# Performance work log

Measured on AMD Instinct MI355X. Metric: run time of the kernel, lower is better.

The kernel has to match this reference:

```python
import jax, jax.numpy as jnp
import numpy as np

B, S, D = 2, 2048, 4096
NQ, NKV, DK = 32, 4, 128
GROUPS = NQ // NKV  # 8
NEG = -1e9  # finite stand-in for -inf so fully-masked rows stay NaN-free


def setup_inputs() -> dict:
    key = jax.random.key(0)
    ks = jax.random.split(key, 5)
    return {
        "x": jax.random.normal(ks[0], (B, S, D), jnp.float32),
        "Wq": jax.random.normal(ks[1], (D, NQ * DK), jnp.float32) * 0.02,
        "Wk": jax.random.normal(ks[2], (D, NKV * DK), jnp.float32) * 0.02,
        "Wv": jax.random.normal(ks[3], (D, NKV * DK), jnp.float32) * 0.02,
        "Wo": jax.random.normal(ks[4], (NQ * DK, D), jnp.float32) * 0.02,
    }


def reference(x, Wq, Wk, Wv, Wo):
    b, s, _ = x.shape
    # projections -> [b, heads, s, dk]
    Q = (x @ Wq).reshape(b, s, NQ, DK).transpose(0, 2, 1, 3)
    K = (x @ Wk).reshape(b, s, NKV, DK).transpose(0, 2, 1, 3)
    V = (x @ Wv).reshape(b, s, NKV, DK).transpose(0, 2, 1, 3)
    # GQA: repeat_interleave KV heads to match Q heads
    K = jnp.repeat(K, GROUPS, axis=1)  # [b, NQ, s, dk]
    V = jnp.repeat(V, GROUPS, axis=1)
    scores = jnp.einsum("bhqd,bhkd->bhqk", Q, K) / np.sqrt(DK).astype(np.float32)
    # faithful to source: mask = triu(ones(s, kv_len), diag=kv_len-s+1); fill where mask==0
    mask = jnp.triu(jnp.ones((s, s), jnp.float32), k=1)
    scores = jnp.where(mask == 0, NEG, scores)
    attn = jax.nn.softmax(scores, axis=-1)  # dropout = identity (eval)
    out = jnp.einsum("bhqk,bhkd->bhqd", attn, V)
    out = out.transpose(0, 2, 1, 3).reshape(b, s, NQ * DK)
    return out @ Wo
```

## Files before the change

kernel.cpp:

```cpp
#include <hip/hip_runtime.h>
#include <hip/hip_bf16.h>

#define S_LEN 2048
#define DMODEL 4096
#define NQH 32
#define NKVH 4
#define DKH 128

typedef __attribute__((ext_vector_type(8))) short bf16x8;
typedef __attribute__((ext_vector_type(4))) float f32x4;
typedef __attribute__((ext_vector_type(16))) float f32x16;
typedef __attribute__((ext_vector_type(2))) unsigned u32x2;

union PU { unsigned u[4]; bf16x8 v; };

__device__ __forceinline__ float b2f(short u) {
  union { float f; unsigned int i; } cv;
  cv.i = ((unsigned int)(unsigned short)u) << 16;
  return cv.f;
}

__device__ __forceinline__ unsigned cvt_pk(float lo, float hi) {
  unsigned r;
  asm("v_cvt_pk_bf16_f32 %0, %1, %2" : "=v"(r) : "v"(lo), "v"(hi));
  return r;
}

__device__ __forceinline__ void gload16(const void* g, void* l) {
  __builtin_amdgcn_global_load_lds(
      (const __attribute__((address_space(1))) void*)g,
      (__attribute__((address_space(3))) void*)l, 16, 0, 0);
}

#define BAR()                         \
  {                                   \
    asm volatile("" ::: "memory");    \
    __builtin_amdgcn_s_barrier();     \
    asm volatile("" ::: "memory");    \
  }

__global__ __launch_bounds__(256) void cast_kernel(
    const float* __restrict__ in, __hip_bfloat16* __restrict__ out, int n4) {
  for (int i = blockIdx.x * 256 + threadIdx.x; i < n4; i += gridDim.x * 256) {
    const float4 v = reinterpret_cast<const float4*>(in)[i];
    __hip_bfloat16 t[4] = {__float2bfloat16(v.x), __float2bfloat16(v.y),
                           __float2bfloat16(v.z), __float2bfloat16(v.w)};
    reinterpret_cast<uint2*>(out)[i] = *reinterpret_cast<const uint2*>(t);
  }
}

__device__ __forceinline__ void transpose_tile(const float* __restrict__ W,
                                               __hip_bfloat16* __restrict__ WT,
                                               int K, int N, int n0, int k0,
                                               int tid,
                                               __hip_bfloat16 (*tile)[64]) {
#pragma unroll
  for (int i = 0; i < 2; ++i) {
    const int fid = i * 256 + tid;
    const int r = fid >> 3, cc = fid & 7;
    const float4 v0 = *reinterpret_cast<const float4*>(
        &W[(size_t)(k0 + r) * N + n0 + cc * 8]);
    const float4 v1 = *reinterpret_cast<const float4*>(
        &W[(size_t)(k0 + r) * N + n0 + cc * 8 + 4]);
    __hip_bfloat16 t[8] = {__float2bfloat16(v0.x), __float2bfloat16(v0.y),
                           __float2bfloat16(v0.z), __float2bfloat16(v0.w),
                           __float2bfloat16(v1.x), __float2bfloat16(v1.y),
                           __float2bfloat16(v1.z), __float2bfloat16(v1.w)};
    *reinterpret_cast<bf16x8*>(&tile[r][(cc ^ (r & 7)) << 3]) =
        *reinterpret_cast<const bf16x8*>(t);
  }
  __syncthreads();
  const int n = tid >> 2, kw = tid & 3;
#pragma unroll
  for (int i = 0; i < 2; ++i) {
    const int kc = kw + i * 4;
    __hip_bfloat16 t[8];
#pragma unroll
    for (int j = 0; j < 8; ++j) {
      const int r = kc * 8 + j;
      t[j] = tile[r][((((n >> 3) ^ (r & 7)) << 3)) + (n & 7)];
    }
    *reinterpret_cast<bf16x8*>(&WT[(size_t)(n0 + n) * K + k0 + kc * 8]) =
        *reinterpret_cast<const bf16x8*>(t);
  }
}

__global__ __launch_bounds__(256) void transpose_cast_kernel(
    const float* __restrict__ W, __hip_bfloat16* __restrict__ WT, int K, int N) {
  __shared__ __align__(16) __hip_bfloat16 tile[64][64];
  transpose_tile(W, WT, K, N, blockIdx.x * 64, blockIdx.y * 64, threadIdx.x,
                 tile);
}

__global__ __launch_bounds__(256) void transpose_kv_kernel(
    const float* __restrict__ Wk, const float* __restrict__ Wv,
    __hip_bfloat16* __restrict__ KVT) {
  __shared__ __align__(16) __hip_bfloat16 tile[64][64];
  const int half = blockIdx.x >> 3;
  const float* W = half ? Wv : Wk;
  __hip_bfloat16* WT = KVT + (size_t)half * 512 * 4096;
  transpose_tile(W, WT, 4096, 512, (blockIdx.x & 7) * 64, blockIdx.y * 64,
                 threadIdx.x, tile);
}

template <int WMODE>
__global__ __launch_bounds__(512, 2) void gemm256(
    const __hip_bfloat16* __restrict__ A, const __hip_bfloat16* __restrict__ BT,
    void* __restrict__ C) {
  __shared__ __align__(16) char ldsA[131072];
  const char* lds = &ldsA[0];
  const int tid = threadIdx.x, lane = tid & 63, w = tid >> 6;
  const int l15 = lane & 15, g = lane >> 4;
  const int wr = w >> 2, wcn = w & 3;
  const int id = blockIdx.x;
  const int swz = (id & 7) * 32 + (id >> 3);
  const int bm = (swz >> 4) * 256, bn = (swz & 15) * 256;
  const int row0 = tid >> 3;
  const int kbg = ((tid & 7) * 16) ^ ((row0 & 7) << 4);
  const char* Ab = (const char*)A;
  const char* Bb = (const char*)BT;
  const size_t aR = (size_t)(bm + row0) * 8192 + kbg;
  const size_t bR = (size_t)(bn + row0) * 8192 + kbg;
  char* ldsw = const_cast<char*>(lds) + w * 1024;
  const int sw = (l15 & 7) << 4;
  const int okk = (g * 16) ^ sw;
  const int rA = (wr * 64 + l15) * 128;
  const int rB = (wcn * 32 + l15) * 128;

  f32x4 acc[8][4] = {};

#define STG2(XR, XB, DST)            \
  gload16(XB + (XR), ldsw + (DST));  \
  gload16(XB + (XR) + 524288, ldsw + (DST) + 8192)

  STG2(aR, Ab, 0);
  STG2(bR, Bb, 65536);
  STG2(aR + 1048576, Ab, 16384);
  STG2(bR + 1048576, Bb, 65536 + 16384);
  STG2(aR + 128, Ab, 32768);
  STG2(bR + 128, Bb, 65536 + 32768);

  for (int t = 0; t < 64; ++t) {
    const int pc = t & 1, pn = pc ^ 1;
    const int pA = pc * 32768, pB = 65536 + pc * 32768;
    const size_t s01 = (size_t)((t + 1 < 64) ? t + 1 : t - 1) * 128;
    const size_t s23 = (size_t)((t + 2 < 64) ? t + 2 : t) * 128;
    asm volatile("s_waitcnt vmcnt(4)" ::: "memory");
    BAR();
    bf16x8 a0[4][2], b0[2][2];
#pragma unroll
    for (int m = 0; m < 4; ++m)
#pragma unroll
      for (int kk = 0; kk < 2; ++kk)
        a0[m][kk] = *reinterpret_cast<const bf16x8*>(
            lds + pA + rA + m * 2048 + (okk ^ (kk << 6)));
#pragma unroll
    for (int n = 0; n < 2; ++n)
#pragma unroll
      for (int kk = 0; kk < 2; ++kk)
        b0[n][kk] = *reinterpret_cast<const bf16x8*>(
            lds + pB + rB + n * 2048 + (okk ^ (kk << 6)));
    STG2(aR + 1048576 + s01, Ab, pn * 32768 + 16384);
    __builtin_amdgcn_s_setprio(1);
#pragma unroll
    for (int kk = 0; kk < 2; ++kk)
#pragma unroll
      for (int m = 0; m < 4; ++m)
#pragma unroll
        for (int n = 0; n < 2; ++n)
          acc[m][n] = __builtin_amdgcn_mfma_f32_16x16x32_bf16(
              a0[m][kk], b0[n][kk], acc[m][n], 0, 0, 0);
    __builtin_amdgcn_s_setprio(0);
    bf16x8 b1[2][2];
#pragma unroll
    for (int n = 0; n < 2; ++n)
#pragma unroll
      for (int kk = 0; kk < 2; ++kk)
        b1[n][kk] = *reinterpret_cast<const bf16x8*>(
            lds + pB + 16384 + rB + n * 2048 + (okk ^ (kk << 6)));
    STG2(bR + 1048576 + s01, Bb, 65536 + pn * 32768 + 16384);
    BAR();
    __builtin_amdgcn_s_setprio(1);
#pragma unroll
    for (int kk = 0; kk < 2; ++kk)
#pragma unroll
      for (int m = 0; m < 4; ++m)
#pragma unroll
        for (int n = 0; n < 2; ++n)
          acc[m][2 + n] = __builtin_amdgcn_mfma_f32_16x16x32_bf16(
              a0[m][kk], b1[n][kk], acc[m][2 + n], 0, 0, 0);
    __builtin_amdgcn_s_setprio(0);
    bf16x8 a1[4][2];
#pragma unroll
    for (int m = 0; m < 4; ++m)
#pragma unroll
      for (int kk = 0; kk < 2; ++kk)
        a1[m][kk] = *reinterpret_cast<const bf16x8*>(
            lds + pA + 16384 + rA + m * 2048 + (okk ^ (kk << 6)));
    STG2(aR + s23, Ab, pc * 32768);
    __builtin_amdgcn_s_setprio(1);
#pragma unroll
    for (int kk = 0; kk < 2; ++kk)
#pragma unroll
      for (int m = 0; m < 4; ++m)
#pragma unroll
        for (int n = 0; n < 2; ++n)
          acc[4 + m][n] = __builtin_amdgcn_mfma_f32_16x16x32_bf16(
              a1[m][kk], b0[n][kk], acc[4 + m][n], 0, 0, 0);
    __builtin_amdgcn_s_setprio(0);
    STG2(bR + s23, Bb, 65536 + pc * 32768);
    __builtin_amdgcn_s_setprio(1);
#pragma unroll
    for (int kk = 0; kk < 2; ++kk)
#pragma unroll
      for (int m = 0; m < 4; ++m)
#pragma unroll
        for (int n = 0; n < 2; ++n)
          acc[4 + m][2 + n] = __builtin_amdgcn_mfma_f32_16x16x32_bf16(
              a1[m][kk], b1[n][kk], acc[4 + m][2 + n], 0, 0, 0);
    __builtin_amdgcn_s_setprio(0);
  }
  asm volatile("s_waitcnt vmcnt(0)" ::: "memory");

  const int crow0 = bm + wr * 64 + g * 4;
  const int ccol0 = bn + wcn * 32 + l15;
#pragma unroll
  for (int M = 0; M < 8; ++M)
#pragma unroll
    for (int N = 0; N < 4; ++N) {
      const int row = crow0 + (M >> 2) * 128 + (M & 3) * 16;
      const int col = ccol0 + (N >> 1) * 128 + (N & 1) * 16;
#pragma unroll
      for (int r = 0; r < 4; ++r) {
        if constexpr (WMODE == 0)
          ((float*)C)[(size_t)(row + r) * 4096 + col] = acc[M][N][r];
        else
          ((__hip_bfloat16*)C)[(size_t)(row + r) * 4096 + col] =
              __float2bfloat16(acc[M][N][r]);
      }
    }
}

__global__ __launch_bounds__(256) void gemm_kv(
    const __hip_bfloat16* __restrict__ A, const __hip_bfloat16* __restrict__ BT,
    __hip_bfloat16* __restrict__ Kb, __hip_bfloat16* __restrict__ VT) {
  __shared__ __align__(16) __hip_bfloat16 As[64 * 32];
  __shared__ __align__(16) __hip_bfloat16 Bs[128 * 32];
  const int tid = threadIdx.x, lane = tid & 63, w = tid >> 6;
  const int l15 = lane & 15, l4 = lane >> 4;
  const int bm = blockIdx.y * 64, bn = blockIdx.x * 128;
  const int wr = (w >> 1) * 32, wc = (w & 1) * 64;
  const int srow = lane >> 2, scol = (lane & 3) * 8;
  const __hip_bfloat16* ga = &A[(size_t)(bm + (tid >> 2)) * 4096 + scol];
  const __hip_bfloat16* gb = &BT[(size_t)(bn + w * 16 + srow) * 4096 + scol];
  char* laA = (char*)&As[0] + w * 1024;
  char* lb0 = (char*)&Bs[0] + w * 1024;
  char* lb1 = (char*)&Bs[0] + 4096 + w * 1024;
  f32x4 acc[2][4] = {};

  for (int k0 = 0; k0 < 4096; k0 += 32) {
    gload16(ga, laA);
    gload16(gb, lb0);
    gload16(gb + (size_t)64 * 4096, lb1);
    ga += 32;
    gb += 32;
    __syncthreads();
    bf16x8 af[2], bfr[4];
#pragma unroll
    for (int m = 0; m < 2; ++m)
      af[m] = *reinterpret_cast<const bf16x8*>(
          &As[(wr + m * 16 + l15) * 32 + l4 * 8]);
#pragma unroll
    for (int n = 0; n < 4; ++n)
      bfr[n] = *reinterpret_cast<const bf16x8*>(
          &Bs[(wc + n * 16 + l15) * 32 + l4 * 8]);
#pragma unroll
    for (int m = 0; m < 2; ++m)
#pragma unroll
      for (int n = 0; n < 4; ++n)
        acc[m][n] = __builtin_amdgcn_mfma_f32_16x16x32_bf16(af[m], bfr[n],
                                                            acc[m][n], 0, 0, 0);
    __syncthreads();
  }

#pragma unroll
  for (int m = 0; m < 2; ++m)
#pragma unroll
    for (int n = 0; n < 4; ++n) {
      const int row = bm + wr + m * 16 + l4 * 4;
      const int col = bn + wc + n * 16 + l15;
      if (col < 512) {
#pragma unroll
        for (int r = 0; r < 4; ++r)
          Kb[(size_t)(row + r) * 512 + col] = __float2bfloat16(acc[m][n][r]);
      } else {
        const int b = row >> 11, s = row & 2047;
        uint2 st;
        st.x = cvt_pk(acc[m][n][0], acc[m][n][1]);
        st.y = cvt_pk(acc[m][n][2], acc[m][n][3]);
        *reinterpret_cast<uint2*>(
            &VT[(size_t)(b * 512 + (col - 512)) * 2048 + s]) = st;
      }
    }
}

__global__ __launch_bounds__(512, 2) void attn_kernel(
    const __hip_bfloat16* __restrict__ Q, const __hip_bfloat16* __restrict__ Kb,
    const __hip_bfloat16* __restrict__ VT, __hip_bfloat16* __restrict__ O) {
  __shared__ __align__(16) __hip_bfloat16 Kbuf[2][64 * 128];
  __shared__ __align__(16) __hip_bfloat16 Vbuf[2][128 * 64];
  const int tid = threadIdx.x, lane = tid & 63, w = tid >> 6;
  const int l31 = lane & 31, h = lane >> 5;
  const int d = blockIdx.x;
  const int xg = d & 7, hh = (d >> 3) & 7, pr = d >> 6;
  const int bh = xg * 8 + hh;
  const int b = bh >> 5, hq = bh & 31, kvh = (bh & 31) >> 3;
  const char* kbase = (const char*)Kb + (size_t)(b * S_LEN) * 1024 + kvh * 256;
  const char* vbase = (const char*)VT + (size_t)(b * 512 + kvh * 128) * 4096;
  const __hip_bfloat16* qbase =
      Q + (size_t)(b * S_LEN) * DMODEL + (size_t)hq * DKH;
  __hip_bfloat16* obase = O + (size_t)(b * S_LEN) * DMODEL + (size_t)hq * DKH;
  const int krr = lane >> 4, kcb = (lane & 15) * 16;
  const int vrr = lane >> 3, vcb = (lane & 7) * 16;
  char* klds = (char*)&Kbuf[0][0] + w * 2048;
  char* vlds = (char*)&Vbuf[0][0] + w * 2048;
  const int swr = (lane & 7) * 16;
  const float SCL2 = 0.12751742f;

  int par = 0;
  for (int ph = 0; ph < 2; ++ph) {
    const int pp = ph ? (7 - pr) : pr;
    const int qw = pp * 256 + w * 32;
    const int qa = qw + l31;
    bf16x8 qf[8];
#pragma unroll
    for (int dkb = 0; dkb < 8; ++dkb)
      qf[dkb] = *reinterpret_cast<const bf16x8*>(
          &qbase[(size_t)qa * DMODEL + dkb * 16 + h * 8]);
    float lsum = 0.f;
    f32x16 oaccT[4] = {};
    const int t0 = pp * 4;
    {
      const int kv0 = t0 * 64;
#pragma unroll
      for (int i = 0; i < 2; ++i) {
        const int rr = 8 * w + 4 * i + krr;
        gload16(kbase + (size_t)(kv0 + rr) * 1024 + (kcb ^ ((rr & 7) * 16)),
                klds + par * 16384 + i * 1024);
        const int r2 = 16 * w + 8 * i + vrr;
        gload16(vbase + (size_t)r2 * 4096 + kv0 * 2 + (vcb ^ ((r2 & 7) * 16)),
                vlds + par * 16384 + i * 1024);
      }
    }
    for (int t = t0; t < 32; ++t) {
      __syncthreads();
      if (t + 1 < 32) {
        const int kv0 = (t + 1) * 64;
        const int np = par ^ 1;
#pragma unroll
        for (int i = 0; i < 2; ++i) {
          const int rr = 8 * w + 4 * i + krr;
          gload16(kbase + (size_t)(kv0 + rr) * 1024 + (kcb ^ ((rr & 7) * 16)),
                  klds + np * 16384 + i * 1024);
          const int r2 = 16 * w + 8 * i + vrr;
          gload16(vbase + (size_t)r2 * 4096 + kv0 * 2 + (vcb ^ ((r2 & 7) * 16)),
                  vlds + np * 16384 + i * 1024);
        }
      }
      const char* kp = (const char*)&Kbuf[0][0] + par * 16384;
      const char* vp = (const char*)&Vbuf[0][0] + par * 16384;
#pragma unroll
      for (int kvb = 0; kvb < 2; ++kvb) {
        f32x16 s = {};
#pragma unroll
        for (int dkb = 0; dkb < 8; ++dkb) {
          const bf16x8 kf = *reinterpret_cast<const bf16x8*>(
              kp + (kvb * 32 + l31) * 256 + ((dkb * 32 + h * 16) ^ swr));
          s = __builtin_amdgcn_mfma_f32_32x32x16_bf16(kf, qf[dkb], s, 0, 0, 0);
        }
#pragma unroll
        for (int r = 0; r < 16; ++r)
          s[r] = __builtin_amdgcn_exp2f(fmaf(s[r], SCL2, -16.f));
        if (t * 64 < qw + 32) {
#pragma unroll
          for (int r = 0; r < 16; ++r) {
            const int kvl = (r & 3) + 8 * (r >> 2) + 4 * h;
            if (t * 64 + kvb * 32 + kvl <= qa) s[r] = 0.f;
          }
        }
#pragma unroll
        for (int r = 0; r < 16; ++r) lsum += s[r];
        unsigned wv[8];
#pragma unroll
        for (int i = 0; i < 8; ++i) wv[i] = cvt_pk(s[2 * i], s[2 * i + 1]);
        const u32x2 s02 =
            __builtin_amdgcn_permlane32_swap(wv[0], wv[2], false, false);
        const u32x2 s13 =
            __builtin_amdgcn_permlane32_swap(wv[1], wv[3], false, false);
        const u32x2 s46 =
            __builtin_amdgcn_permlane32_swap(wv[4], wv[6], false, false);
        const u32x2 s57 =
            __builtin_amdgcn_permlane32_swap(wv[5], wv[7], false, false);
        PU pb1, pb2;
        pb1.u[0] = s02[0]; pb1.u[1] = s13[0]; pb1.u[2] = s02[1]; pb1.u[3] = s13[1];
        pb2.u[0] = s46[0]; pb2.u[1] = s57[0]; pb2.u[2] = s46[1]; pb2.u[3] = s57[1];
#pragma unroll
        for (int dkblk = 0; dkblk < 4; ++dkblk) {
          const bf16x8 vf1 = *reinterpret_cast<const bf16x8*>(
              vp + (dkblk * 32 + l31) * 128 + ((kvb * 64 + h * 16) ^ swr));
          oaccT[dkblk] = __builtin_amdgcn_mfma_f32_32x32x16_bf16(
              vf1, pb1.v, oaccT[dkblk], 0, 0, 0);
          const bf16x8 vf2 = *reinterpret_cast<const bf16x8*>(
              vp + (dkblk * 32 + l31) * 128 + ((kvb * 64 + 32 + h * 16) ^ swr));
          oaccT[dkblk] = __builtin_amdgcn_mfma_f32_32x32x16_bf16(
              vf2, pb2.v, oaccT[dkblk], 0, 0, 0);
        }
      }
      par ^= 1;
    }
    lsum += __shfl_xor(lsum, 32);
    const float rinv = 1.f / lsum;
    __hip_bfloat16* orow = obase + (size_t)qa * DMODEL;
#pragma unroll
    for (int dkblk = 0; dkblk < 4; ++dkblk)
#pragma unroll
      for (int b4 = 0; b4 < 4; ++b4) {
        uint2 st;
        st.x = cvt_pk(oaccT[dkblk][4 * b4 + 0] * rinv,
                      oaccT[dkblk][4 * b4 + 1] * rinv);
        st.y = cvt_pk(oaccT[dkblk][4 * b4 + 2] * rinv,
                      oaccT[dkblk][4 * b4 + 3] * rinv);
        *reinterpret_cast<uint2*>(&orow[dkblk * 32 + b4 * 8 + 4 * h]) = st;
      }
    __syncthreads();
  }
}

__global__ __launch_bounds__(128) void fixup_kernel(
    const __hip_bfloat16* __restrict__ VT, __hip_bfloat16* __restrict__ O) {
  const int b = blockIdx.x >> 5;
  const int h = blockIdx.x & 31;
  const int kvh = h >> 3;
  const int dk = threadIdx.x;
  const __hip_bfloat16* row = &VT[(size_t)(b * 512 + kvh * DKH + dk) * S_LEN];
  float s = 0.f;
  for (int i = 0; i < S_LEN / 8; ++i) {
    const bf16x8 v = *reinterpret_cast<const bf16x8*>(&row[i * 8]);
#pragma unroll
    for (int j = 0; j < 8; ++j) s += b2f(v[j]);
  }
  O[(size_t)(b * S_LEN + S_LEN - 1) * DMODEL + h * DKH + dk] =
      __float2bfloat16(s * (1.f / S_LEN));
}

extern "C" void kernel_launch(void* const* d_in, const int* in_sizes, int n_in,
                              void* d_out, int out_size, void* d_ws,
                              size_t ws_size, hipStream_t stream) {
  (void)in_sizes; (void)n_in; (void)out_size; (void)ws_size;
  const float* x = (const float*)d_in[0];
  const float* Wq = (const float*)d_in[1];
  const float* Wk = (const float*)d_in[2];
  const float* Wv = (const float*)d_in[3];
  const float* Wo = (const float*)d_in[4];
  float* out = (float*)d_out;

  char* ws = (char*)d_ws;
  __hip_bfloat16* xb  = (__hip_bfloat16*)(ws + 0);
  __hip_bfloat16* WT0 = (__hip_bfloat16*)(ws + 33554432ull);
  __hip_bfloat16* KVT = (__hip_bfloat16*)(ws + 67108864ull);
  __hip_bfloat16* Qb  = (__hip_bfloat16*)(ws + 75497472ull);
  __hip_bfloat16* Kb  = (__hip_bfloat16*)(ws + 109051904ull);
  __hip_bfloat16* VT  = (__hip_bfloat16*)(ws + 113246208ull);
  __hip_bfloat16* AO  = xb;

  const int M = 2 * S_LEN;
  dim3 blk(256);

  cast_kernel<<<dim3(2048), blk, 0, stream>>>(x, xb, (M * DMODEL) / 4);
  transpose_cast_kernel<<<dim3(64, 64), blk, 0, stream>>>(Wq, WT0, DMODEL, DMODEL);
  gemm256<1><<<dim3(256), dim3(512), 0, stream>>>(xb, WT0, Qb);
  transpose_kv_kernel<<<dim3(16, 64), blk, 0, stream>>>(Wk, Wv, KVT);
  gemm_kv<<<dim3(8, 64), blk, 0, stream>>>(xb, KVT, Kb, VT);
  attn_kernel<<<dim3(256), dim3(512), 0, stream>>>(Qb, Kb, VT, AO);
  fixup_kernel<<<dim3(64), dim3(128), 0, stream>>>(VT, AO);
  transpose_cast_kernel<<<dim3(64, 64), blk, 0, stream>>>(Wo, WT0, DMODEL, DMODEL);
  gemm256<0><<<dim3(256), dim3(512), 0, stream>>>(AO, WT0, out);
}
```

Before: 440.5 us.

## Triple-buffer LDS in gemm_kv with async prefetch two tiles ahead

Converts the K/V projection GEMM from a single-buffered load-sync-compute-sync loop to a three-stage LDS ring. Global-to-LDS loads are issued two k-tiles ahead, and a vmcnt wait plus one barrier per iteration replaces the two __syncthreads. This hides global load latency behind MFMA work at the cost of three times the LDS footprint. The last iterations reload a valid tile instead of going out of bounds.

```diff
diff --git a/kernel.cpp b/kernel.cpp
--- a/kernel.cpp
+++ b/kernel.cpp
@@ -244,44 +244,56 @@
 __global__ __launch_bounds__(256) void gemm_kv(
     const __hip_bfloat16* __restrict__ A, const __hip_bfloat16* __restrict__ BT,
     __hip_bfloat16* __restrict__ Kb, __hip_bfloat16* __restrict__ VT) {
-  __shared__ __align__(16) __hip_bfloat16 As[64 * 32];
-  __shared__ __align__(16) __hip_bfloat16 Bs[128 * 32];
+  __shared__ __align__(16) char ldsb[3][12288];
+  char* ldsbase = &ldsb[0][0];
   const int tid = threadIdx.x, lane = tid & 63, w = tid >> 6;
   const int l15 = lane & 15, l4 = lane >> 4;
   const int bm = blockIdx.y * 64, bn = blockIdx.x * 128;
   const int wr = (w >> 1) * 32, wc = (w & 1) * 64;
   const int srow = lane >> 2, scol = (lane & 3) * 8;
-  const __hip_bfloat16* ga = &A[(size_t)(bm + (tid >> 2)) * 4096 + scol];
-  const __hip_bfloat16* gb = &BT[(size_t)(bn + w * 16 + srow) * 4096 + scol];
-  char* laA = (char*)&As[0] + w * 1024;
-  char* lb0 = (char*)&Bs[0] + w * 1024;
-  char* lb1 = (char*)&Bs[0] + 4096 + w * 1024;
+  const char* ga = (const char*)&A[(size_t)(bm + (tid >> 2)) * 4096 + scol];
+  const char* gb =
+      (const char*)&BT[(size_t)(bn + w * 16 + srow) * 4096 + scol];
   f32x4 acc[2][4] = {};
 
-  for (int k0 = 0; k0 < 4096; k0 += 32) {
-    gload16(ga, laA);
-    gload16(gb, lb0);
-    gload16(gb + (size_t)64 * 4096, lb1);
-    ga += 32;
-    gb += 32;
-    __syncthreads();
+#define KVSTG(T, BUF)                                                   \
+  {                                                                     \
+    const size_t ko = (size_t)(T) * 64;                                 \
+    gload16(ga + ko, ldsbase + (BUF) * 12288 + w * 1024);               \
+    gload16(gb + ko, ldsbase + (BUF) * 12288 + 4096 + w * 1024);        \
+    gload16(gb + 524288 + ko, ldsbase + (BUF) * 12288 + 8192 + w * 1024); \
+  }
+
+  KVSTG(0, 0);
+  KVSTG(1, 1);
+  int cur = 0;
+  for (int t = 0; t < 128; ++t) {
+    asm volatile("s_waitcnt vmcnt(3)" ::: "memory");
+    BAR();
+    const char* bp = ldsbase + cur * 12288;
     bf16x8 af[2], bfr[4];
 #pragma unroll
     for (int m = 0; m < 2; ++m)
       af[m] = *reinterpret_cast<const bf16x8*>(
-          &As[(wr + m * 16 + l15) * 32 + l4 * 8]);
+          bp + (wr + m * 16 + l15) * 64 + l4 * 16);
 #pragma unroll
     for (int n = 0; n < 4; ++n)
       bfr[n] = *reinterpret_cast<const bf16x8*>(
-          &Bs[(wc + n * 16 + l15) * 32 + l4 * 8]);
+          bp + 4096 + (wc + n * 16 + l15) * 64 + l4 * 16);
+    const int t2 = (t + 2 < 128) ? t + 2 : t;
+    int b2 = cur + 2;
+    if (b2 >= 3) b2 -= 3;
+    KVSTG(t2, b2);
 #pragma unroll
     for (int m = 0; m < 2; ++m)
 #pragma unroll
       for (int n = 0; n < 4; ++n)
         acc[m][n] = __builtin_amdgcn_mfma_f32_16x16x32_bf16(af[m], bfr[n],
                                                             acc[m][n], 0, 0, 0);
-    __syncthreads();
-  }
+    ++cur;
+    if (cur == 3) cur = 0;
+  }
+  asm volatile("s_waitcnt vmcnt(0)" ::: "memory");
 
 #pragma unroll
   for (int m = 0; m < 2; ++m)
```

Measured after the change: 428.2 us, median of 2. 1.03x faster.
